# Kernel tuning notes

Measured on AMD Instinct MI355X. Metric: run time of the kernel, lower is better.

Reference implementation:

```python
import jax, jax.numpy as jnp
import numpy as np

B, T, E, H = 2, 2048, 1024, 16
D = E // H  # head dim = 64


def setup_inputs() -> dict:
    key = jax.random.key(0)
    kx, kq, kk, kv, kw = jax.random.split(key, 5)
    # kaiming-normal-like init for per-head projections, xavier-like for output proj
    qkv_std = (2.0 / E) ** 0.5
    w_std = (6.0 / (E + E)) ** 0.5 / (3.0 ** 0.5)
    x = jax.random.normal(kx, (B, T, E), dtype=jnp.float32)
    Wq = jax.random.normal(kq, (H, E, D), dtype=jnp.float32) * qkv_std
    Wk = jax.random.normal(kk, (H, E, D), dtype=jnp.float32) * qkv_std
    Wv = jax.random.normal(kv, (H, E, D), dtype=jnp.float32) * qkv_std
    Wo = jax.random.normal(kw, (E, E), dtype=jnp.float32) * w_std
    return {"x": x, "Wq": Wq, "Wk": Wk, "Wv": Wv, "Wo": Wo}


def reference(x, Wq, Wk, Wv, Wo):
    # per-head projections, batched over heads: bte,hed->bhtd
    q = jnp.einsum('bte,hed->bhtd', x, Wq)
    k = jnp.einsum('bte,hed->bhtd', x, Wk)
    v = jnp.einsum('bte,hed->bhtd', x, Wv)
    scale = 1.0 / jnp.sqrt(jnp.asarray(D, dtype=q.dtype))
    scores = jnp.einsum('bhtd,bhTd->bhtT', q, k) * scale  # [B,H,T,T]
    attn = jax.nn.softmax(scores, axis=-1)
    heads = jnp.einsum('bhtT,bhTd->bhtd', attn, v)  # [B,H,T,D]
    # concat heads along feature dim (head order preserved)
    combined = heads.transpose(0, 2, 1, 3).reshape(B, T, E)
    return combined @ Wo + x
```

## Files before the change

kernel.cpp:

```cpp
#include <hip/hip_runtime.h>
#include <hip/hip_bf16.h>


#define B_ 2
#define T_ 2048
#define E_ 1024
#define H_ 16
#define D_ 64
#define VTS_ 2176
#define LD_ 72

typedef _Float16 h8 __attribute__((ext_vector_type(8)));
typedef _Float16 h4 __attribute__((ext_vector_type(4)));
typedef float f32x4 __attribute__((ext_vector_type(4)));

union U4 { uint4 u; h8 h; };

__device__ __forceinline__ float h2f(unsigned short s) {
  _Float16 h;
  __builtin_memcpy(&h, &s, 2);
  return (float)h;
}

__device__ __forceinline__ unsigned short f2h(float f) {
  _Float16 h = (_Float16)f;
  unsigned short s;
  __builtin_memcpy(&s, &h, 2);
  return s;
}

__global__ __launch_bounds__(256) void cvt_x(const float* __restrict__ x,
                                             unsigned short* __restrict__ xh) {
  const size_t i = ((size_t)blockIdx.x * 256 + threadIdx.x) * 4;
  const float4 f = *(const float4*)(x + i);
  ushort4 pk;
  pk.x = f2h(f.x); pk.y = f2h(f.y); pk.z = f2h(f.z); pk.w = f2h(f.w);
  *(ushort4*)(xh + i) = pk;
}

__global__ __launch_bounds__(256) void tconv_w(
    const float* __restrict__ Wq, const float* __restrict__ Wk,
    const float* __restrict__ Wv, unsigned short* __restrict__ wt) {
  __shared__ float ts[64][65];
  const int p = blockIdx.z, h = blockIdx.y;
  const float* src = ((p == 0) ? Wq : (p == 1) ? Wk : Wv) + (size_t)h * E_ * D_;
  unsigned short* dst = wt + (size_t)(p * H_ + h) * D_ * E_;
  const int r0 = blockIdx.x * 64;
  const int lr = threadIdx.x >> 4, lc = (threadIdx.x & 15) * 4;
#pragma unroll
  for (int it = 0; it < 4; it++) {
    const float4 f = *(const float4*)(src + (size_t)(r0 + lr + it * 16) * D_ + lc);
    ts[lr + it * 16][lc] = f.x; ts[lr + it * 16][lc + 1] = f.y;
    ts[lr + it * 16][lc + 2] = f.z; ts[lr + it * 16][lc + 3] = f.w;
  }
  __syncthreads();
#pragma unroll
  for (int it = 0; it < 4; it++) {
    const int dr = lr + it * 16;
    ushort4 pk;
    pk.x = f2h(ts[lc + 0][dr]); pk.y = f2h(ts[lc + 1][dr]);
    pk.z = f2h(ts[lc + 2][dr]); pk.w = f2h(ts[lc + 3][dr]);
    *(ushort4*)(dst + (size_t)dr * E_ + r0 + lc) = pk;
  }
}

__global__ __launch_bounds__(256) void tconv_wo(const float* __restrict__ Wo,
                                                unsigned short* __restrict__ wot) {
  __shared__ float ts[64][65];
  const int r0 = blockIdx.x * 64;
  const int c0 = blockIdx.y * 64;
  const int lr = threadIdx.x >> 4, lc = (threadIdx.x & 15) * 4;
#pragma unroll
  for (int it = 0; it < 4; it++) {
    const float4 f = *(const float4*)(Wo + (size_t)(r0 + lr + it * 16) * E_ + c0 + lc);
    ts[lr + it * 16][lc] = f.x; ts[lr + it * 16][lc + 1] = f.y;
    ts[lr + it * 16][lc + 2] = f.z; ts[lr + it * 16][lc + 3] = f.w;
  }
  __syncthreads();
#pragma unroll
  for (int it = 0; it < 4; it++) {
    const int dr = lr + it * 16;
    ushort4 pk;
    pk.x = f2h(ts[lc + 0][dr]); pk.y = f2h(ts[lc + 1][dr]);
    pk.z = f2h(ts[lc + 2][dr]); pk.w = f2h(ts[lc + 3][dr]);
    *(ushort4*)(wot + (size_t)(c0 + dr) * E_ + r0 + lc) = pk;
  }
}

__global__ __launch_bounds__(256) void qkv_mfma(
    const unsigned short* __restrict__ xh, const unsigned short* __restrict__ wt,
    unsigned short* __restrict__ qo, unsigned short* __restrict__ ko,
    unsigned short* __restrict__ vo)
{
  __shared__ unsigned short xs[128 * LD_];
  __shared__ unsigned short wsb[64 * LD_];
  __shared__ unsigned short Cl[4][32 * 72];

  const int tid = threadIdx.x;
  const int w = tid >> 6, lane = tid & 63;
  const int m16 = lane & 15, quad = lane >> 4;
  const int h = blockIdx.y, p = blockIdx.z;
  const int n0 = blockIdx.x * 128;
  const unsigned short* wb = wt + (size_t)(p * H_ + h) * D_ * E_;

  const int sr = tid >> 3;
  const int sc = (tid & 7) * 8;

  f32x4 acc[2][4];
#pragma unroll
  for (int rt = 0; rt < 2; rt++)
#pragma unroll
    for (int ct = 0; ct < 4; ct++) acc[rt][ct] = (f32x4){0.f, 0.f, 0.f, 0.f};

  for (int e0 = 0; e0 < E_; e0 += 64) {
    __syncthreads();
#pragma unroll
    for (int it = 0; it < 4; it++) {
      const int row = it * 32 + sr;
      *(uint4*)(xs + row * LD_ + sc) =
          *(const uint4*)(xh + (size_t)(n0 + row) * E_ + e0 + sc);
    }
#pragma unroll
    for (int it = 0; it < 2; it++) {
      const int row = it * 32 + sr;
      *(uint4*)(wsb + row * LD_ + sc) =
          *(const uint4*)(wb + (size_t)row * E_ + e0 + sc);
    }
    __syncthreads();

#pragma unroll
    for (int kk = 0; kk < 64; kk += 32) {
      U4 a0, a1, bf[4];
      a0.u = *(const uint4*)(xs + (w * 32 + m16) * LD_ + kk + quad * 8);
      a1.u = *(const uint4*)(xs + (w * 32 + 16 + m16) * LD_ + kk + quad * 8);
#pragma unroll
      for (int ct = 0; ct < 4; ct++)
        bf[ct].u = *(const uint4*)(wsb + (ct * 16 + m16) * LD_ + kk + quad * 8);
#pragma unroll
      for (int ct = 0; ct < 4; ct++) {
        acc[0][ct] = __builtin_amdgcn_mfma_f32_16x16x32_f16(a0.h, bf[ct].h, acc[0][ct], 0, 0, 0);
        acc[1][ct] = __builtin_amdgcn_mfma_f32_16x16x32_f16(a1.h, bf[ct].h, acc[1][ct], 0, 0, 0);
      }
    }
  }

  const int nw = n0 + w * 32;
  const int b  = n0 >> 11;
  const int t0 = nw & (T_ - 1);
  const size_t bh = (size_t)(b * H_ + h);

  if (p == 2) {
#pragma unroll
    for (int rt = 0; rt < 2; rt++)
#pragma unroll
      for (int ct = 0; ct < 4; ct++) {
        const int d = ct * 16 + m16;
        const int t = t0 + rt * 16 + quad * 4;
        ushort4 pk;
        pk.x = f2h(acc[rt][ct][0]); pk.y = f2h(acc[rt][ct][1]);
        pk.z = f2h(acc[rt][ct][2]); pk.w = f2h(acc[rt][ct][3]);
        *(ushort4*)(vo + (bh * D_ + d) * (size_t)VTS_ + t) = pk;
      }
  } else {
    unsigned short* outp = (p == 0) ? qo : ko;
    unsigned short* Cw = &Cl[w][0];
#pragma unroll
    for (int rt = 0; rt < 2; rt++)
#pragma unroll
      for (int ct = 0; ct < 4; ct++)
#pragma unroll
        for (int r = 0; r < 4; r++)
          Cw[(rt * 16 + quad * 4 + r) * 72 + ct * 16 + m16] = f2h(acc[rt][ct][r]);
    const int row = lane >> 1;
    const int half = (lane & 1) * 32;
    const uint4 d0 = *(const uint4*)(Cw + row * 72 + half);
    const uint4 d1 = *(const uint4*)(Cw + row * 72 + half + 8);
    const uint4 d2 = *(const uint4*)(Cw + row * 72 + half + 16);
    const uint4 d3 = *(const uint4*)(Cw + row * 72 + half + 24);
    unsigned short* dst = outp + (bh * T_ + t0 + row) * D_ + half;
    *(uint4*)(dst)      = d0;
    *(uint4*)(dst + 8)  = d1;
    *(uint4*)(dst + 16) = d2;
    *(uint4*)(dst + 24) = d3;
  }
}

__global__ __launch_bounds__(256) void attn_kernel(
    const unsigned short* __restrict__ q, const unsigned short* __restrict__ k,
    const unsigned short* __restrict__ vt, unsigned short* __restrict__ comb)
{
  __shared__ unsigned short Kt[2][64 * LD_];
  __shared__ unsigned short Vt[2][64 * LD_];

  const int tid  = threadIdx.x;
  const int w    = tid >> 6;
  const int lane = tid & 63;
  const int m16  = lane & 15;
  const int quad = lane >> 4;
  const int h = blockIdx.y, b = blockIdx.z;
  const size_t bh = (size_t)(b * H_ + h);
  const int q0 = blockIdx.x * 64 + w * 16;

  U4 aQ0, aQ1;
  {
    const unsigned short* qrow = q + (bh * T_ + q0 + m16) * (size_t)D_;
    aQ0.u = *(const uint4*)(qrow + quad * 8);
    aQ1.u = *(const uint4*)(qrow + 32 + quad * 8);
    aQ0.h = aQ0.h * (_Float16)0.125f;
    aQ1.h = aQ1.h * (_Float16)0.125f;
  }

  f32x4 o0 = {0.f, 0.f, 0.f, 0.f}, o1 = o0, o2 = o0, o3 = o0;
  float mrow = -1e30f;
  float lrow = 0.f;

  const unsigned short* kb  = k  + bh * (size_t)(T_ * D_);
  const unsigned short* vtb = vt + bh * (size_t)(D_ * VTS_);

  const int sr = tid >> 3;
  const int sc = (tid & 7) * 8;

  uint4 kr0, kr1, vr0, vr1;
  kr0 = *(const uint4*)(kb + (size_t)sr * D_ + sc);
  kr1 = *(const uint4*)(kb + (size_t)(32 + sr) * D_ + sc);
  vr0 = *(const uint4*)(vtb + (size_t)sr * VTS_ + sc);
  vr1 = *(const uint4*)(vtb + (size_t)(32 + sr) * VTS_ + sc);
  *(uint4*)(&Kt[0][0] + sr * LD_ + sc)        = kr0;
  *(uint4*)(&Kt[0][0] + (32 + sr) * LD_ + sc) = kr1;
  *(uint4*)(&Vt[0][0] + sr * LD_ + sc)        = vr0;
  *(uint4*)(&Vt[0][0] + (32 + sr) * LD_ + sc) = vr1;
  __syncthreads();

  const int NT = T_ / 64;
  for (int t = 0; t < NT; t++) {
    const int cur = t & 1;
    const unsigned short* Kc = &Kt[cur][0];
    const unsigned short* Vc = &Vt[cur][0];
    const bool more = (t + 1 < NT);
    if (more) {
      const int kt = (t + 1) * 64;
      kr0 = *(const uint4*)(kb + (size_t)(kt + sr) * D_ + sc);
      kr1 = *(const uint4*)(kb + (size_t)(kt + 32 + sr) * D_ + sc);
      vr0 = *(const uint4*)(vtb + (size_t)sr * VTS_ + kt + sc);
      vr1 = *(const uint4*)(vtb + (size_t)(32 + sr) * VTS_ + kt + sc);
    }

    f32x4 st[4];
#pragma unroll
    for (int ct = 0; ct < 4; ct++) {
      U4 kf0, kf1;
      kf0.u = *(const uint4*)(Kc + (ct * 16 + m16) * LD_ + quad * 8);
      kf1.u = *(const uint4*)(Kc + (ct * 16 + m16) * LD_ + 32 + quad * 8);
      f32x4 z = {0.f, 0.f, 0.f, 0.f};
      z = __builtin_amdgcn_mfma_f32_16x16x32_f16(kf0.h, aQ0.h, z, 0, 0, 0);
      z = __builtin_amdgcn_mfma_f32_16x16x32_f16(kf1.h, aQ1.h, z, 0, 0, 0);
      st[ct] = z;
    }

    const float m0 = fmaxf(fmaxf(st[0][0], st[0][1]), fmaxf(st[0][2], st[0][3]));
    const float m1 = fmaxf(fmaxf(st[1][0], st[1][1]), fmaxf(st[1][2], st[1][3]));
    const float m2 = fmaxf(fmaxf(st[2][0], st[2][1]), fmaxf(st[2][2], st[2][3]));
    const float m3 = fmaxf(fmaxf(st[3][0], st[3][1]), fmaxf(st[3][2], st[3][3]));
    float ml = fmaxf(fmaxf(m0, m1), fmaxf(m2, m3));
    ml = fmaxf(ml, __shfl_xor(ml, 16));
    ml = fmaxf(ml, __shfl_xor(ml, 32));

    const float mn = fmaxf(mrow, ml);
    const float a  = __expf(mrow - mn);
    mrow = mn;

    float sl = 0.f;
    h4 pf[4];
#pragma unroll
    for (int ct = 0; ct < 4; ct++) {
      const float e0 = __expf(st[ct][0] - mn);
      const float e1 = __expf(st[ct][1] - mn);
      const float e2 = __expf(st[ct][2] - mn);
      const float e3 = __expf(st[ct][3] - mn);
      sl += (e0 + e1) + (e2 + e3);
      pf[ct] = (h4){(_Float16)e0, (_Float16)e1, (_Float16)e2, (_Float16)e3};
    }
    sl += __shfl_xor(sl, 16);
    sl += __shfl_xor(sl, 32);
    lrow = lrow * a + sl;

    float al[4];
#pragma unroll
    for (int r = 0; r < 4; r++) al[r] = __shfl(a, quad * 4 + r);
#pragma unroll
    for (int r = 0; r < 4; r++) {
      o0[r] *= al[r]; o1[r] *= al[r]; o2[r] *= al[r]; o3[r] *= al[r];
    }

#pragma unroll
    for (int ctd = 0; ctd < 4; ctd++) {
      f32x4* op = (ctd == 0) ? &o0 : (ctd == 1) ? &o1 : (ctd == 2) ? &o2 : &o3;
      const unsigned short* vrw = Vc + (ctd * 16 + m16) * LD_ + quad * 4;
#pragma unroll
      for (int ctk = 0; ctk < 4; ctk++) {
        const h4 vf = *(const h4*)(vrw + ctk * 16);
        *op = __builtin_amdgcn_mfma_f32_16x16x16f16(pf[ctk], vf, *op, 0, 0, 0);
      }
    }

    if (more) {
      __syncthreads();
      unsigned short* Kn = &Kt[cur ^ 1][0];
      unsigned short* Vn = &Vt[cur ^ 1][0];
      *(uint4*)(Kn + sr * LD_ + sc)        = kr0;
      *(uint4*)(Kn + (32 + sr) * LD_ + sc) = kr1;
      *(uint4*)(Vn + sr * LD_ + sc)        = vr0;
      *(uint4*)(Vn + (32 + sr) * LD_ + sc) = vr1;
      __syncthreads();
    }
  }

  float linv[4];
#pragma unroll
  for (int r = 0; r < 4; r++) linv[r] = 1.f / __shfl(lrow, quad * 4 + r);

#pragma unroll
  for (int r = 0; r < 4; r++) {
    const int tq = q0 + quad * 4 + r;
    unsigned short* dst = comb + ((size_t)b * T_ + tq) * E_ + h * D_;
    dst[m16]      = f2h(o0[r] * linv[r]);
    dst[16 + m16] = f2h(o1[r] * linv[r]);
    dst[32 + m16] = f2h(o2[r] * linv[r]);
    dst[48 + m16] = f2h(o3[r] * linv[r]);
  }
}

__global__ __launch_bounds__(256) void out_mfma(
    const unsigned short* __restrict__ comb, const unsigned short* __restrict__ wot,
    const float* __restrict__ x, float* __restrict__ out)
{
  __shared__ unsigned short cs[128 * LD_];
  __shared__ unsigned short wsb[64 * LD_];

  const int tid = threadIdx.x;
  const int w = tid >> 6, lane = tid & 63;
  const int m16 = lane & 15, quad = lane >> 4;
  const int n0 = blockIdx.x * 128;
  const int j0 = blockIdx.y * 64;

  const int sr = tid >> 3;
  const int sc = (tid & 7) * 8;

  f32x4 acc[2][4];
#pragma unroll
  for (int rt = 0; rt < 2; rt++)
#pragma unroll
    for (int ct = 0; ct < 4; ct++) acc[rt][ct] = (f32x4){0.f, 0.f, 0.f, 0.f};

  for (int e0 = 0; e0 < E_; e0 += 64) {
    __syncthreads();
#pragma unroll
    for (int it = 0; it < 4; it++) {
      const int row = it * 32 + sr;
      *(uint4*)(cs + row * LD_ + sc) =
          *(const uint4*)(comb + (size_t)(n0 + row) * E_ + e0 + sc);
    }
#pragma unroll
    for (int it = 0; it < 2; it++) {
      const int row = it * 32 + sr;
      *(uint4*)(wsb + row * LD_ + sc) =
          *(const uint4*)(wot + (size_t)(j0 + row) * E_ + e0 + sc);
    }
    __syncthreads();

#pragma unroll
    for (int kk = 0; kk < 64; kk += 32) {
      U4 a0, a1, bf[4];
      a0.u = *(const uint4*)(cs + (w * 32 + m16) * LD_ + kk + quad * 8);
      a1.u = *(const uint4*)(cs + (w * 32 + 16 + m16) * LD_ + kk + quad * 8);
#pragma unroll
      for (int ct = 0; ct < 4; ct++)
        bf[ct].u = *(const uint4*)(wsb + (ct * 16 + m16) * LD_ + kk + quad * 8);
#pragma unroll
      for (int ct = 0; ct < 4; ct++) {
        acc[0][ct] = __builtin_amdgcn_mfma_f32_16x16x32_f16(a0.h, bf[ct].h, acc[0][ct], 0, 0, 0);
        acc[1][ct] = __builtin_amdgcn_mfma_f32_16x16x32_f16(a1.h, bf[ct].h, acc[1][ct], 0, 0, 0);
      }
    }
  }

  const int nw = n0 + w * 32;
#pragma unroll
  for (int rt = 0; rt < 2; rt++)
#pragma unroll
    for (int r = 0; r < 4; r++) {
      const int n = nw + rt * 16 + quad * 4 + r;
      const float* xr = x + (size_t)n * E_ + j0;
      float* orow = out + (size_t)n * E_ + j0;
#pragma unroll
      for (int ct = 0; ct < 4; ct++) {
        const int j = ct * 16 + m16;
        orow[j] = acc[rt][ct][r] + xr[j];
      }
    }
}

extern "C" void kernel_launch(void* const* d_in, const int* in_sizes, int n_in,
                              void* d_out, int out_size, void* d_ws, size_t ws_size,
                              hipStream_t stream) {
  (void)in_sizes; (void)n_in; (void)out_size; (void)ws_size;

  const float* x  = (const float*)d_in[0];
  const float* Wq = (const float*)d_in[1];
  const float* Wk = (const float*)d_in[2];
  const float* Wv = (const float*)d_in[3];
  const float* Wo = (const float*)d_in[4];
  float* out = (float*)d_out;

  unsigned short* ws0  = (unsigned short*)d_ws;
  unsigned short* xh   = ws0;
  unsigned short* wt   = ws0 + 4194304;
  unsigned short* wot  = ws0 + 7340032;
  unsigned short* qh   = ws0 + 8388608;
  unsigned short* kh   = ws0 + 12582912;
  unsigned short* vth  = ws0 + 16777216;
  unsigned short* comb = xh;

  cvt_x<<<dim3(B_ * T_ * E_ / 1024), dim3(256), 0, stream>>>(x, xh);
  tconv_w<<<dim3(E_ / 64, H_, 3), dim3(256), 0, stream>>>(Wq, Wk, Wv, wt);
  tconv_wo<<<dim3(E_ / 64, E_ / 64), dim3(256), 0, stream>>>(Wo, wot);

  qkv_mfma<<<dim3(B_ * T_ / 128, H_, 3), dim3(256), 0, stream>>>(xh, wt, qh, kh, vth);

  attn_kernel<<<dim3(T_ / 64, H_, B_), dim3(256), 0, stream>>>(qh, kh, vth, comb);

  out_mfma<<<dim3(B_ * T_ / 128, E_ / 64), dim3(256), 0, stream>>>(comb, wot, x, out);
}
```

Measured before the change: 224.4 us.

## Enlarge attention KV tile to 128, add lazy rescaling and block swizzle

The attention kernel now processes 128 keys per iteration using a single LDS buffer staged through registers, which halves the number of barrier-separated iterations. The V prefetch is split to issue after the QK MFMAs. The online-softmax rescale of the output accumulators is skipped unless some row max grows by more than 8. Softmax probabilities are packed to fp16 with the cvt_pkrtz instruction. The grid is flattened to 1D with an XCD-aware swizzle so blocks sharing a (b,h) land on the same XCD, and launch bounds request 4 waves per SIMD. The costs are higher register pressure, a round-toward-zero conversion of the probabilities, and thresholded rescaling that lets the unnormalized exponentials grow up to e^8 in fp16 and fp32.

```diff
diff --git a/kernel.cpp b/kernel.cpp
--- a/kernel.cpp
+++ b/kernel.cpp
@@ -9,12 +9,18 @@
 #define D_ 64
 #define VTS_ 2176
 #define LD_ 72
+#define KV_ 128
+#define LDK_ 72
+#define LDV_ 144
+#define NTILE_ (T_ / KV_)
 
 typedef _Float16 h8 __attribute__((ext_vector_type(8)));
 typedef _Float16 h4 __attribute__((ext_vector_type(4)));
+typedef __fp16  pk2 __attribute__((ext_vector_type(2)));
 typedef float f32x4 __attribute__((ext_vector_type(4)));
 
 union U4 { uint4 u; h8 h; };
+union PK4 { pk2 p[2]; h4 h; };
 
 __device__ __forceinline__ float h2f(unsigned short s) {
   _Float16 h;
@@ -185,21 +191,27 @@
   }
 }
 
-__global__ __launch_bounds__(256) void attn_kernel(
+__global__ __launch_bounds__(256, 4) void attn_kernel(
     const unsigned short* __restrict__ q, const unsigned short* __restrict__ k,
     const unsigned short* __restrict__ vt, unsigned short* __restrict__ comb)
 {
-  __shared__ unsigned short Kt[2][64 * LD_];
-  __shared__ unsigned short Vt[2][64 * LD_];
+  __shared__ unsigned short Kt[KV_ * LDK_];
+  __shared__ unsigned short Vt[D_ * LDV_];
 
   const int tid  = threadIdx.x;
   const int w    = tid >> 6;
   const int lane = tid & 63;
   const int m16  = lane & 15;
   const int quad = lane >> 4;
-  const int h = blockIdx.y, b = blockIdx.z;
+
+  const int flat = blockIdx.x;
+  const int swz  = (flat & 7) * 128 + (flat >> 3);
+  const int xq   = swz & 31;
+  const int h    = (swz >> 5) & 15;
+  const int b    = swz >> 9;
+
   const size_t bh = (size_t)(b * H_ + h);
-  const int q0 = blockIdx.x * 64 + w * 16;
+  const int q0 = xq * 64 + w * 16;
 
   U4 aQ0, aQ1;
   {
@@ -214,103 +226,114 @@
   float mrow = -1e30f;
   float lrow = 0.f;
 
-  const unsigned short* kb  = k  + bh * (size_t)(T_ * D_);
-  const unsigned short* vtb = vt + bh * (size_t)(D_ * VTS_);
-
-  const int sr = tid >> 3;
-  const int sc = (tid & 7) * 8;
-
-  uint4 kr0, kr1, vr0, vr1;
-  kr0 = *(const uint4*)(kb + (size_t)sr * D_ + sc);
-  kr1 = *(const uint4*)(kb + (size_t)(32 + sr) * D_ + sc);
-  vr0 = *(const uint4*)(vtb + (size_t)sr * VTS_ + sc);
-  vr1 = *(const uint4*)(vtb + (size_t)(32 + sr) * VTS_ + sc);
-  *(uint4*)(&Kt[0][0] + sr * LD_ + sc)        = kr0;
-  *(uint4*)(&Kt[0][0] + (32 + sr) * LD_ + sc) = kr1;
-  *(uint4*)(&Vt[0][0] + sr * LD_ + sc)        = vr0;
-  *(uint4*)(&Vt[0][0] + (32 + sr) * LD_ + sc) = vr1;
+  const int sr = tid >> 3, sc = (tid & 7) * 8;
+  const int vr2 = tid >> 4, vc = (tid & 15) * 8;
+
+  const unsigned short* kp = k  + bh * (size_t)(T_ * D_)   + sr * D_ + sc;
+  const unsigned short* vp = vt + bh * (size_t)(D_ * VTS_) + vr2 * VTS_ + vc;
+  unsigned short* ksw = Kt + sr * LDK_ + sc;
+  unsigned short* vsw = Vt + vr2 * LDV_ + vc;
+
+  uint4 krg[4], vrg[4];
+#pragma unroll
+  for (int i = 0; i < 4; i++) krg[i] = *(const uint4*)(kp + i * 32 * D_);
+#pragma unroll
+  for (int i = 0; i < 4; i++) vrg[i] = *(const uint4*)(vp + i * 16 * VTS_);
+  kp += KV_ * D_; vp += KV_;
+#pragma unroll
+  for (int i = 0; i < 4; i++) *(uint4*)(ksw + i * 32 * LDK_) = krg[i];
+#pragma unroll
+  for (int i = 0; i < 4; i++) *(uint4*)(vsw + i * 16 * LDV_) = vrg[i];
   __syncthreads();
 
-  const int NT = T_ / 64;
-  for (int t = 0; t < NT; t++) {
-    const int cur = t & 1;
-    const unsigned short* Kc = &Kt[cur][0];
-    const unsigned short* Vc = &Vt[cur][0];
-    const bool more = (t + 1 < NT);
+  const unsigned short* Kw = Kt + m16 * LDK_ + quad * 8;
+  const unsigned short* Vw = Vt + m16 * LDV_ + quad * 4;
+
+  for (int t = 0; t < NTILE_; t++) {
+    const bool more = (t + 1 < NTILE_);
     if (more) {
-      const int kt = (t + 1) * 64;
-      kr0 = *(const uint4*)(kb + (size_t)(kt + sr) * D_ + sc);
-      kr1 = *(const uint4*)(kb + (size_t)(kt + 32 + sr) * D_ + sc);
-      vr0 = *(const uint4*)(vtb + (size_t)sr * VTS_ + kt + sc);
-      vr1 = *(const uint4*)(vtb + (size_t)(32 + sr) * VTS_ + kt + sc);
-    }
-
-    f32x4 st[4];
-#pragma unroll
-    for (int ct = 0; ct < 4; ct++) {
+#pragma unroll
+      for (int i = 0; i < 4; i++) krg[i] = *(const uint4*)(kp + i * 32 * D_);
+      kp += KV_ * D_;
+    }
+
+    f32x4 st[8];
+#pragma unroll
+    for (int ct = 0; ct < 8; ct++) {
       U4 kf0, kf1;
-      kf0.u = *(const uint4*)(Kc + (ct * 16 + m16) * LD_ + quad * 8);
-      kf1.u = *(const uint4*)(Kc + (ct * 16 + m16) * LD_ + 32 + quad * 8);
+      kf0.u = *(const uint4*)(Kw + ct * 16 * LDK_);
+      kf1.u = *(const uint4*)(Kw + ct * 16 * LDK_ + 32);
       f32x4 z = {0.f, 0.f, 0.f, 0.f};
       z = __builtin_amdgcn_mfma_f32_16x16x32_f16(kf0.h, aQ0.h, z, 0, 0, 0);
       z = __builtin_amdgcn_mfma_f32_16x16x32_f16(kf1.h, aQ1.h, z, 0, 0, 0);
       st[ct] = z;
     }
 
-    const float m0 = fmaxf(fmaxf(st[0][0], st[0][1]), fmaxf(st[0][2], st[0][3]));
-    const float m1 = fmaxf(fmaxf(st[1][0], st[1][1]), fmaxf(st[1][2], st[1][3]));
-    const float m2 = fmaxf(fmaxf(st[2][0], st[2][1]), fmaxf(st[2][2], st[2][3]));
-    const float m3 = fmaxf(fmaxf(st[3][0], st[3][1]), fmaxf(st[3][2], st[3][3]));
-    float ml = fmaxf(fmaxf(m0, m1), fmaxf(m2, m3));
+    if (more) {
+#pragma unroll
+      for (int i = 0; i < 4; i++) vrg[i] = *(const uint4*)(vp + i * 16 * VTS_);
+      vp += KV_;
+    }
+
+    float ml = fmaxf(fmaxf(st[0][0], st[0][1]), fmaxf(st[0][2], st[0][3]));
+#pragma unroll
+    for (int ct = 1; ct < 8; ct++) {
+      const float mc = fmaxf(fmaxf(st[ct][0], st[ct][1]), fmaxf(st[ct][2], st[ct][3]));
+      ml = fmaxf(ml, mc);
+    }
     ml = fmaxf(ml, __shfl_xor(ml, 16));
     ml = fmaxf(ml, __shfl_xor(ml, 32));
 
-    const float mn = fmaxf(mrow, ml);
-    const float a  = __expf(mrow - mn);
-    mrow = mn;
+    if (!__all(ml - mrow <= 8.0f)) {
+      const float mn = fmaxf(mrow, ml);
+      const float a  = __expf(mrow - mn);
+      float al[4];
+#pragma unroll
+      for (int r = 0; r < 4; r++) al[r] = __shfl(a, quad * 4 + r);
+#pragma unroll
+      for (int r = 0; r < 4; r++) {
+        o0[r] *= al[r]; o1[r] *= al[r]; o2[r] *= al[r]; o3[r] *= al[r];
+      }
+      lrow *= a;
+      mrow = mn;
+    }
+    const float mn = mrow;
 
     float sl = 0.f;
-    h4 pf[4];
-#pragma unroll
-    for (int ct = 0; ct < 4; ct++) {
+    h4 pf[8];
+#pragma unroll
+    for (int ct = 0; ct < 8; ct++) {
       const float e0 = __expf(st[ct][0] - mn);
       const float e1 = __expf(st[ct][1] - mn);
       const float e2 = __expf(st[ct][2] - mn);
       const float e3 = __expf(st[ct][3] - mn);
       sl += (e0 + e1) + (e2 + e3);
-      pf[ct] = (h4){(_Float16)e0, (_Float16)e1, (_Float16)e2, (_Float16)e3};
+      PK4 u;
+      u.p[0] = __builtin_amdgcn_cvt_pkrtz(e0, e1);
+      u.p[1] = __builtin_amdgcn_cvt_pkrtz(e2, e3);
+      pf[ct] = u.h;
     }
     sl += __shfl_xor(sl, 16);
     sl += __shfl_xor(sl, 32);
-    lrow = lrow * a + sl;
-
-    float al[4];
-#pragma unroll
-    for (int r = 0; r < 4; r++) al[r] = __shfl(a, quad * 4 + r);
-#pragma unroll
-    for (int r = 0; r < 4; r++) {
-      o0[r] *= al[r]; o1[r] *= al[r]; o2[r] *= al[r]; o3[r] *= al[r];
-    }
+    lrow += sl;
 
 #pragma unroll
     for (int ctd = 0; ctd < 4; ctd++) {
       f32x4* op = (ctd == 0) ? &o0 : (ctd == 1) ? &o1 : (ctd == 2) ? &o2 : &o3;
-      const unsigned short* vrw = Vc + (ctd * 16 + m16) * LD_ + quad * 4;
-#pragma unroll
-      for (int ctk = 0; ctk < 4; ctk++) {
-        const h4 vf = *(const h4*)(vrw + ctk * 16);
+      const unsigned short* vrow = Vw + ctd * 16 * LDV_;
+#pragma unroll
+      for (int ctk = 0; ctk < 8; ctk++) {
+        const h4 vf = *(const h4*)(vrow + ctk * 16);
         *op = __builtin_amdgcn_mfma_f32_16x16x16f16(pf[ctk], vf, *op, 0, 0, 0);
       }
     }
 
+    __syncthreads();
     if (more) {
-      __syncthreads();
-      unsigned short* Kn = &Kt[cur ^ 1][0];
-      unsigned short* Vn = &Vt[cur ^ 1][0];
-      *(uint4*)(Kn + sr * LD_ + sc)        = kr0;
-      *(uint4*)(Kn + (32 + sr) * LD_ + sc) = kr1;
-      *(uint4*)(Vn + sr * LD_ + sc)        = vr0;
-      *(uint4*)(Vn + (32 + sr) * LD_ + sc) = vr1;
+#pragma unroll
+      for (int i = 0; i < 4; i++) *(uint4*)(ksw + i * 32 * LDK_) = krg[i];
+#pragma unroll
+      for (int i = 0; i < 4; i++) *(uint4*)(vsw + i * 16 * LDV_) = vrg[i];
       __syncthreads();
     }
   }
@@ -427,7 +450,7 @@
 
   qkv_mfma<<<dim3(B_ * T_ / 128, H_, 3), dim3(256), 0, stream>>>(xh, wt, qh, kh, vth);
 
-  attn_kernel<<<dim3(T_ / 64, H_, B_), dim3(256), 0, stream>>>(qh, kh, vth, comb);
+  attn_kernel<<<dim3(B_ * H_ * (T_ / 64)), dim3(256), 0, stream>>>(qh, kh, vth, comb);
 
   out_mfma<<<dim3(B_ * T_ / 128, E_ / 64), dim3(256), 0, stream>>>(comb, wot, x, out);
 }
```

After: 302.8 us. 1.35x slower.

## Skip online-softmax rescale with threshold and swizzle attention grid across XCDs

Applied to the files above, without the earlier changes.

Switches the attention kernel's online softmax to a lazy rescale. The running max and the accumulator/denominator rescale are updated only when some row's new tile max exceeds the stored max by more than 8, so most iterations skip the exp, shuffles and 16 multiplies. The launch grid is flattened to 1D and remapped so that consecutive block IDs, which are dispatched round-robin across XCDs, give each XCD contiguous (b,h) groups for better K/V L2 reuse. The lazy rescale lets unnormalized exponentials reach up to e^8 before conversion to fp16, which stays in range but changes rounding slightly.

```diff
diff --git a/kernel.cpp b/kernel.cpp
--- a/kernel.cpp
+++ b/kernel.cpp
@@ -197,9 +197,15 @@
   const int lane = tid & 63;
   const int m16  = lane & 15;
   const int quad = lane >> 4;
-  const int h = blockIdx.y, b = blockIdx.z;
+
+  const int flat = blockIdx.x;
+  const int swz  = (flat & 7) * 128 + (flat >> 3);
+  const int xq   = swz & 31;
+  const int h    = (swz >> 5) & 15;
+  const int b    = swz >> 9;
+
   const size_t bh = (size_t)(b * H_ + h);
-  const int q0 = blockIdx.x * 64 + w * 16;
+  const int q0 = xq * 64 + w * 16;
 
   U4 aQ0, aQ1;
   {
@@ -210,7 +216,9 @@
     aQ1.h = aQ1.h * (_Float16)0.125f;
   }
 
-  f32x4 o0 = {0.f, 0.f, 0.f, 0.f}, o1 = o0, o2 = o0, o3 = o0;
+  f32x4 o[4];
+#pragma unroll
+  for (int i = 0; i < 4; i++) o[i] = (f32x4){0.f, 0.f, 0.f, 0.f};
   float mrow = -1e30f;
   float lrow = 0.f;
 
@@ -265,9 +273,20 @@
     ml = fmaxf(ml, __shfl_xor(ml, 16));
     ml = fmaxf(ml, __shfl_xor(ml, 32));
 
-    const float mn = fmaxf(mrow, ml);
-    const float a  = __expf(mrow - mn);
-    mrow = mn;
+    if (!__all(ml - mrow <= 8.0f)) {
+      const float mn2 = fmaxf(mrow, ml);
+      const float a   = __expf(mrow - mn2);
+      float al[4];
+#pragma unroll
+      for (int r = 0; r < 4; r++) al[r] = __shfl(a, quad * 4 + r);
+#pragma unroll
+      for (int i = 0; i < 4; i++)
+#pragma unroll
+        for (int r = 0; r < 4; r++) o[i][r] *= al[r];
+      lrow *= a;
+      mrow = mn2;
+    }
+    const float mn = mrow;
 
     float sl = 0.f;
     h4 pf[4];
@@ -282,24 +301,15 @@
     }
     sl += __shfl_xor(sl, 16);
     sl += __shfl_xor(sl, 32);
-    lrow = lrow * a + sl;
-
-    float al[4];
-#pragma unroll
-    for (int r = 0; r < 4; r++) al[r] = __shfl(a, quad * 4 + r);
-#pragma unroll
-    for (int r = 0; r < 4; r++) {
-      o0[r] *= al[r]; o1[r] *= al[r]; o2[r] *= al[r]; o3[r] *= al[r];
-    }
+    lrow += sl;
 
 #pragma unroll
     for (int ctd = 0; ctd < 4; ctd++) {
-      f32x4* op = (ctd == 0) ? &o0 : (ctd == 1) ? &o1 : (ctd == 2) ? &o2 : &o3;
-      const unsigned short* vrw = Vc + (ctd * 16 + m16) * LD_ + quad * 4;
+      const unsigned short* vrow = Vc + (ctd * 16 + m16) * LD_ + quad * 4;
 #pragma unroll
       for (int ctk = 0; ctk < 4; ctk++) {
-        const h4 vf = *(const h4*)(vrw + ctk * 16);
-        *op = __builtin_amdgcn_mfma_f32_16x16x16f16(pf[ctk], vf, *op, 0, 0, 0);
+        const h4 vf = *(const h4*)(vrow + ctk * 16);
+        o[ctd] = __builtin_amdgcn_mfma_f32_16x16x16f16(pf[ctk], vf, o[ctd], 0, 0, 0);
       }
     }
 
@@ -323,10 +333,10 @@
   for (int r = 0; r < 4; r++) {
     const int tq = q0 + quad * 4 + r;
     unsigned short* dst = comb + ((size_t)b * T_ + tq) * E_ + h * D_;
-    dst[m16]      = f2h(o0[r] * linv[r]);
-    dst[16 + m16] = f2h(o1[r] * linv[r]);
-    dst[32 + m16] = f2h(o2[r] * linv[r]);
-    dst[48 + m16] = f2h(o3[r] * linv[r]);
+    dst[m16]      = f2h(o[0][r] * linv[r]);
+    dst[16 + m16] = f2h(o[1][r] * linv[r]);
+    dst[32 + m16] = f2h(o[2][r] * linv[r]);
+    dst[48 + m16] = f2h(o[3][r] * linv[r]);
   }
 }
 
@@ -427,7 +437,7 @@
 
   qkv_mfma<<<dim3(B_ * T_ / 128, H_, 3), dim3(256), 0, stream>>>(xh, wt, qh, kh, vth);
 
-  attn_kernel<<<dim3(T_ / 64, H_, B_), dim3(256), 0, stream>>>(qh, kh, vth, comb);
+  attn_kernel<<<dim3(B_ * H_ * (T_ / 64)), dim3(256), 0, stream>>>(qh, kh, vth, comb);
 
   out_mfma<<<dim3(B_ * T_ / 128, E_ / 64), dim3(256), 0, stream>>>(comb, wot, x, out);
 }
```

Result: no change. 221.4 us (-1.3%).
